# Kernel tuning notes

Hardware: AMD Instinct MI355X
Metric: run time of the kernel (lower is better)

The kernel has to match this reference:

```python
import jax, jax.numpy as jnp
import numpy as np

B, T, IN_DIM, EMB = 8, 2048, 1024, 1024
NEG_INF = -1e30  # stand-in for float('-inf'); exp() underflows to 0 identically


def setup_inputs() -> dict:
    key = jax.random.key(0)
    ks = jax.random.split(key, 7)
    s = 1.0 / np.sqrt(IN_DIM)
    return {
        "x": jax.random.normal(ks[0], (B, T, IN_DIM), dtype=jnp.float32),
        "Wq": jax.random.normal(ks[1], (IN_DIM, EMB), dtype=jnp.float32) * s,
        "bq": jax.random.normal(ks[2], (EMB,), dtype=jnp.float32) * 0.01,
        "Wk": jax.random.normal(ks[3], (IN_DIM, EMB), dtype=jnp.float32) * s,
        "bk": jax.random.normal(ks[4], (EMB,), dtype=jnp.float32) * 0.01,
        "Wv": jax.random.normal(ks[5], (IN_DIM, EMB), dtype=jnp.float32) * s,
        "bv": jax.random.normal(ks[6], (EMB,), dtype=jnp.float32) * 0.01,
    }


def reference(x, Wq, bq, Wk, bk, Wv, bv):
    # projections: [B, T, EMB]
    q = x @ Wq + bq
    k = x @ Wk + bk
    v = x @ Wv + bv
    scale = jnp.asarray(EMB, x.dtype) ** 0.5
    # scores: [B, T, T]
    scores = jnp.einsum("btd,bsd->bts", q, k) / scale
    Tq = scores.shape[-2]
    causal = jnp.tril(jnp.ones((Tq, Tq), dtype=bool))  # [T, T]
    scores = jnp.where(causal, scores, jnp.asarray(NEG_INF, scores.dtype))
    # Faithful to torch.vmap(softmax): per-batch GLOBAL-matrix softmax
    # (max and sum taken over the whole [T, T] matrix, not per row).
    m = jnp.max(scores, axis=(-2, -1), keepdims=True)
    e = jnp.exp(scores - m)
    w = e / jnp.sum(e, axis=(-2, -1), keepdims=True)
    # output: [B, T, EMB]
    return jnp.einsum("bts,bsd->btd", w, v)
```

## Files before the change

### kernel.cpp

```cpp
#include <hip/hip_runtime.h>
#include <stdint.h>


#define B_   8
#define T_   2048
#define DIM  1024

typedef _Float16 f16;
typedef f16   f16x8 __attribute__((ext_vector_type(8)));
typedef f16   f16x4 __attribute__((ext_vector_type(4)));
typedef float f32x4 __attribute__((ext_vector_type(4)));

typedef const __attribute__((address_space(1))) void gvoid_t;
typedef __attribute__((address_space(3))) void lvoid_t;


__device__ __forceinline__ void stage_half256(const uint16_t* __restrict__ g, int ld,
                                              uint16_t* s, int tid) {
#pragma unroll
  for (int j = 0; j < 2; ++j) {
    int r   = j * 64 + (tid >> 3);
    int seg = (tid & 7) ^ (r & 7);
    const uint16_t* gp = g + (size_t)r * ld + seg * 8;
    uint16_t* sp = s + j * 4096 + (tid >> 6) * 512;
    __builtin_amdgcn_global_load_lds((gvoid_t*)gp, (lvoid_t*)sp, 16, 0, 0);
  }
}

__device__ __forceinline__ f16x8 frag64(const uint16_t* s, int r, int gseg) {
  return *(const f16x8*)(s + r * 64 + ((gseg ^ (r & 7)) * 8));
}

__device__ __forceinline__ void lda4(const uint16_t* s, int rbase, int quad, int l15,
                                     f16x8 o[4][2]) {
#pragma unroll
  for (int mf = 0; mf < 4; ++mf) {
    int r = rbase + mf * 16 + l15;
#pragma unroll
    for (int kk = 0; kk < 2; ++kk) o[mf][kk] = frag64(s, r, kk * 4 + quad);
  }
}

__device__ __forceinline__ void ldb2(const uint16_t* s, int rbase, int quad, int l15,
                                     f16x8 o[2][2]) {
#pragma unroll
  for (int nf = 0; nf < 2; ++nf) {
    int r = rbase + nf * 16 + l15;
#pragma unroll
    for (int kk = 0; kk < 2; ++kk) o[nf][kk] = frag64(s, r, kk * 4 + quad);
  }
}

__device__ __forceinline__ void ldb1(const uint16_t* s, int rbase, int quad, int l15,
                                     f16x8 o[2]) {
  int r = rbase + l15;
#pragma unroll
  for (int kk = 0; kk < 2; ++kk) o[kk] = frag64(s, r, kk * 4 + quad);
}

template <int M0, int N0>
__device__ __forceinline__ void mm16(f16x8 a[4][2], f16x8 b[2][2], f32x4 (&acc)[8][4]) {
#pragma unroll
  for (int kk = 0; kk < 2; ++kk)
#pragma unroll
    for (int mf = 0; mf < 4; ++mf)
#pragma unroll
      for (int nf = 0; nf < 2; ++nf)
        acc[M0 + mf][N0 + nf] = __builtin_amdgcn_mfma_f32_16x16x32_f16(
            a[mf][kk], b[nf][kk], acc[M0 + mf][N0 + nf], 0, 0, 0);
}

template <int M0, int N0>
__device__ __forceinline__ void mm8(f16x8 a[4][2], f16x8 b[2], f32x4 (&acc)[8][2]) {
#pragma unroll
  for (int kk = 0; kk < 2; ++kk)
#pragma unroll
    for (int mf = 0; mf < 4; ++mf)
      acc[M0 + mf][N0] = __builtin_amdgcn_mfma_f32_16x16x32_f16(
          a[mf][kk], b[kk], acc[M0 + mf][N0], 0, 0, 0);
}

#define SYNC_MFMA(AA, BB, M0, N0)                      \
  __builtin_amdgcn_s_barrier();                        \
  asm volatile("s_waitcnt lgkmcnt(0)" ::: "memory");   \
  __builtin_amdgcn_s_setprio(1);                       \
  mm16<M0, N0>(AA, BB, acc);                           \
  __builtin_amdgcn_s_setprio(0);                       \
  __builtin_amdgcn_s_barrier();

#define SYNC_MFMA8(AA, BB, M0, N0)                     \
  __builtin_amdgcn_s_barrier();                        \
  asm volatile("s_waitcnt lgkmcnt(0)" ::: "memory");   \
  __builtin_amdgcn_s_setprio(1);                       \
  mm8<M0, N0>(AA, BB, acc);                            \
  __builtin_amdgcn_s_setprio(0);                       \
  __builtin_amdgcn_s_barrier();

__device__ __forceinline__ void gemm256_8ph(const uint16_t* __restrict__ gA,
                                            const uint16_t* __restrict__ gB,
                                            int lda, int ldb, int nIter,
                                            uint16_t* smem, f32x4 (&acc)[8][4]) {
  const int tid = threadIdx.x, lane = tid & 63;
  const int quad = lane >> 4, l15 = lane & 15;
  const int wv = tid >> 6, wr = wv >> 2, wc = wv & 3;

  uint16_t* sA0 = smem;
  uint16_t* sA1 = smem + 16384;
  uint16_t* sB0 = smem + 32768;
  uint16_t* sB1 = smem + 49152;

  stage_half256(gA,                          lda, sA0,        tid);
  stage_half256(gA + 128 * (size_t)lda,      lda, sA0 + 8192, tid);
  stage_half256(gB,                          ldb, sB0,        tid);
  stage_half256(gB + 128 * (size_t)ldb,      ldb, sB0 + 8192, tid);
  stage_half256(gB + 64,                     ldb, sB1,        tid);
  stage_half256(gB + 64 + 128 * (size_t)ldb, ldb, sB1 + 8192, tid);
  asm volatile("s_waitcnt vmcnt(4)" ::: "memory");
  __builtin_amdgcn_s_barrier();

  f16x8 alo[4][2], ahi[4][2], blo[2][2], bhi[2][2];
#pragma unroll 1
  for (int it = 0; it < nIter - 1; ++it) {
    const int t1 = 2 * it + 1, t2 = 2 * it + 2, t3 = 2 * it + 3;
    const uint16_t* gA1 = gA + t1 * 64;
    const uint16_t* gA2 = gA + t2 * 64;
    const uint16_t* gB2 = gB + t2 * 64;
    const uint16_t* gB3 = gB + t3 * 64;

    lda4(sA0, wr * 128,      quad, l15, alo);
    ldb2(sB0, wc * 64,       quad, l15, blo);
    stage_half256(gA1, lda, sA1, tid);
    SYNC_MFMA(alo, blo, 0, 0)
    ldb2(sB0, wc * 64 + 32,  quad, l15, bhi);
    stage_half256(gA1 + 128 * (size_t)lda, lda, sA1 + 8192, tid);
    SYNC_MFMA(alo, bhi, 0, 2)
    lda4(sA0, wr * 128 + 64, quad, l15, ahi);
    stage_half256(gB2, ldb, sB0, tid);
    SYNC_MFMA(ahi, bhi, 4, 2)
    stage_half256(gB2 + 128 * (size_t)ldb, ldb, sB0 + 8192, tid);
    asm volatile("s_waitcnt vmcnt(4)" ::: "memory");
    SYNC_MFMA(ahi, blo, 4, 0)
    lda4(sA1, wr * 128,      quad, l15, alo);
    ldb2(sB1, wc * 64,       quad, l15, blo);
    stage_half256(gA2, lda, sA0, tid);
    SYNC_MFMA(alo, blo, 0, 0)
    ldb2(sB1, wc * 64 + 32,  quad, l15, bhi);
    stage_half256(gA2 + 128 * (size_t)lda, lda, sA0 + 8192, tid);
    SYNC_MFMA(alo, bhi, 0, 2)
    lda4(sA1, wr * 128 + 64, quad, l15, ahi);
    stage_half256(gB3, ldb, sB1, tid);
    SYNC_MFMA(ahi, bhi, 4, 2)
    stage_half256(gB3 + 128 * (size_t)ldb, ldb, sB1 + 8192, tid);
    asm volatile("s_waitcnt vmcnt(4)" ::: "memory");
    SYNC_MFMA(ahi, blo, 4, 0)
  }

  {
    const uint16_t* gA1 = gA + (2 * nIter - 1) * 64;
    lda4(sA0, wr * 128,      quad, l15, alo);
    ldb2(sB0, wc * 64,       quad, l15, blo);
    stage_half256(gA1, lda, sA1, tid);
    SYNC_MFMA(alo, blo, 0, 0)
    ldb2(sB0, wc * 64 + 32,  quad, l15, bhi);
    stage_half256(gA1 + 128 * (size_t)lda, lda, sA1 + 8192, tid);
    SYNC_MFMA(alo, bhi, 0, 2)
    lda4(sA0, wr * 128 + 64, quad, l15, ahi);
    SYNC_MFMA(ahi, bhi, 4, 2)
    asm volatile("s_waitcnt vmcnt(0)" ::: "memory");
    SYNC_MFMA(ahi, blo, 4, 0)
    lda4(sA1, wr * 128,      quad, l15, alo);
    ldb2(sB1, wc * 64,       quad, l15, blo);
    SYNC_MFMA(alo, blo, 0, 0)
    ldb2(sB1, wc * 64 + 32,  quad, l15, bhi);
    SYNC_MFMA(alo, bhi, 0, 2)
    lda4(sA1, wr * 128 + 64, quad, l15, ahi);
    SYNC_MFMA(ahi, bhi, 4, 2)
    SYNC_MFMA(ahi, blo, 4, 0)
  }
}

__device__ __forceinline__ void gemm256n128_8ph(const uint16_t* __restrict__ gA,
                                                const uint16_t* __restrict__ gB,
                                                int lda, int ldb, int nIter,
                                                uint16_t* smem, f32x4 (&acc)[8][2]) {
  const int tid = threadIdx.x, lane = tid & 63;
  const int quad = lane >> 4, l15 = lane & 15;
  const int wv = tid >> 6, wr = wv >> 2, wc = wv & 3;

  uint16_t* sA0 = smem;
  uint16_t* sA1 = smem + 16384;
  uint16_t* sB0 = smem + 32768;
  uint16_t* sB1 = smem + 40960;

  stage_half256(gA,                     lda, sA0,        tid);
  stage_half256(gA + 128 * (size_t)lda, lda, sA0 + 8192, tid);
  stage_half256(gB,                     ldb, sB0,        tid);
  stage_half256(gB + 64,                ldb, sB1,        tid);
  asm volatile("s_waitcnt vmcnt(2)" ::: "memory");
  __builtin_amdgcn_s_barrier();

  f16x8 alo[4][2], ahi[4][2], b0[2], b1[2];
#pragma unroll 1
  for (int it = 0; it < nIter - 1; ++it) {
    const int t1 = 2 * it + 1, t2 = 2 * it + 2, t3 = 2 * it + 3;
    const uint16_t* gA1 = gA + t1 * 64;
    const uint16_t* gA2 = gA + t2 * 64;

    lda4(sA0, wr * 128,      quad, l15, alo);
    ldb1(sB0, wc * 32,       quad, l15, b0);
    stage_half256(gA1, lda, sA1, tid);
    SYNC_MFMA8(alo, b0, 0, 0)
    ldb1(sB0, wc * 32 + 16,  quad, l15, b1);
    stage_half256(gA1 + 128 * (size_t)lda, lda, sA1 + 8192, tid);
    SYNC_MFMA8(alo, b1, 0, 1)
    lda4(sA0, wr * 128 + 64, quad, l15, ahi);
    stage_half256(gB + t2 * 64, ldb, sB0, tid);
    SYNC_MFMA8(ahi, b1, 4, 1)
    asm volatile("s_waitcnt vmcnt(2)" ::: "memory");
    SYNC_MFMA8(ahi, b0, 4, 0)
    lda4(sA1, wr * 128,      quad, l15, alo);
    ldb1(sB1, wc * 32,       quad, l15, b0);
    stage_half256(gA2, lda, sA0, tid);
    SYNC_MFMA8(alo, b0, 0, 0)
    ldb1(sB1, wc * 32 + 16,  quad, l15, b1);
    stage_half256(gA2 + 128 * (size_t)lda, lda, sA0 + 8192, tid);
    SYNC_MFMA8(alo, b1, 0, 1)
    lda4(sA1, wr * 128 + 64, quad, l15, ahi);
    stage_half256(gB + t3 * 64, ldb, sB1, tid);
    SYNC_MFMA8(ahi, b1, 4, 1)
    asm volatile("s_waitcnt vmcnt(2)" ::: "memory");
    SYNC_MFMA8(ahi, b0, 4, 0)
  }

  {
    const uint16_t* gA1 = gA + (2 * nIter - 1) * 64;
    lda4(sA0, wr * 128,      quad, l15, alo);
    ldb1(sB0, wc * 32,       quad, l15, b0);
    stage_half256(gA1, lda, sA1, tid);
    SYNC_MFMA8(alo, b0, 0, 0)
    ldb1(sB0, wc * 32 + 16,  quad, l15, b1);
    stage_half256(gA1 + 128 * (size_t)lda, lda, sA1 + 8192, tid);
    SYNC_MFMA8(alo, b1, 0, 1)
    lda4(sA0, wr * 128 + 64, quad, l15, ahi);
    SYNC_MFMA8(ahi, b1, 4, 1)
    asm volatile("s_waitcnt vmcnt(0)" ::: "memory");
    SYNC_MFMA8(ahi, b0, 4, 0)
    lda4(sA1, wr * 128,      quad, l15, alo);
    ldb1(sB1, wc * 32,       quad, l15, b0);
    SYNC_MFMA8(alo, b0, 0, 0)
    ldb1(sB1, wc * 32 + 16,  quad, l15, b1);
    SYNC_MFMA8(alo, b1, 0, 1)
    lda4(sA1, wr * 128 + 64, quad, l15, ahi);
    SYNC_MFMA8(ahi, b1, 4, 1)
    SYNC_MFMA8(ahi, b0, 4, 0)
  }
}

__device__ __forceinline__ void zero_acc8(f32x4 (&acc)[8][4]) {
  f32x4 z = {0.f, 0.f, 0.f, 0.f};
#pragma unroll
  for (int i = 0; i < 8; ++i)
#pragma unroll
    for (int j = 0; j < 4; ++j) acc[i][j] = z;
}


__global__ void zero_lrow_kernel(float* __restrict__ lrow) {
  lrow[blockIdx.x * 256 + threadIdx.x] = 0.f;
}

__global__ void conv_x_kernel(const float* __restrict__ x, f16* __restrict__ xf) {
  size_t i = (size_t)blockIdx.x * 256 + threadIdx.x;
  float4 v = ((const float4*)x)[i];
  f16x4 o = {(f16)v.x, (f16)v.y, (f16)v.z, (f16)v.w};
  ((f16x4*)xf)[i] = o;
}

__global__ void convT_w_kernel(const float* __restrict__ Wq, const float* __restrict__ Wk,
                               const float* __restrict__ Wv, f16* __restrict__ WT) {
  __shared__ float tile[64][65];
  const int z = blockIdx.z;
  const float* W = (z == 0) ? Wq : (z == 1) ? Wk : Wv;
  const int r0 = blockIdx.x * 64, c0 = blockIdx.y * 64, tid = threadIdx.x;
#pragma unroll
  for (int i = 0; i < 16; ++i) {
    int rr = (tid >> 6) + 4 * i, cc = tid & 63;
    tile[rr][cc] = W[(size_t)(r0 + rr) * DIM + c0 + cc];
  }
  __syncthreads();
#pragma unroll
  for (int i = 0; i < 16; ++i) {
    int nn = (tid >> 6) + 4 * i, kk = tid & 63;
    WT[(size_t)z * DIM * DIM + (size_t)(c0 + nn) * DIM + r0 + kk] = (f16)tile[kk][nn];
  }
}

__global__ void reduce_z_kernel(const float* __restrict__ lrow, float* __restrict__ invZ) {
  const int b = blockIdx.x, tid = threadIdx.x;
  float s = 0.f;
  for (int i = tid; i < T_; i += 256) s += lrow[(size_t)b * T_ + i];
#pragma unroll
  for (int off = 1; off < 64; off <<= 1) s += __shfl_xor(s, off, 64);
  __shared__ float red[4];
  if ((tid & 63) == 0) red[tid >> 6] = s;
  __syncthreads();
  if (tid == 0) invZ[b] = 1.0f / (red[0] + red[1] + red[2] + red[3]);
}


__global__ __launch_bounds__(512, 2) void proj_kernel(
    const f16* __restrict__ xf, const f16* __restrict__ WT,
    const float* __restrict__ bq, const float* __restrict__ bk, const float* __restrict__ bv,
    f16* __restrict__ q, f16* __restrict__ k, f16* __restrict__ vT) {
  __shared__ uint16_t smem[65536];

  const int bid = blockIdx.x;
  const int xcd = bid & 7, local = bid >> 3;
  const int bx = xcd * 8 + (local & 7);
  const int zy = local >> 3;
  const int z = zy >> 2, by = zy & 3;
  const size_t arow = (size_t)bx * 256;
  const int    bcol = by * 256;

  f32x4 acc[8][4];
  zero_acc8(acc);
  gemm256_8ph((const uint16_t*)xf + arow * DIM,
              (const uint16_t*)WT + (size_t)z * DIM * DIM + (size_t)bcol * DIM,
              DIM, DIM, 8, smem, acc);

  const float* bias = (z == 0) ? bq : (z == 1) ? bk : bv;
  const int tid = threadIdx.x, lane = tid & 63, wv = tid >> 6;
  const int quad = lane >> 4, l15 = lane & 15;
  const int wr = wv >> 2, wc = wv & 3;
  if (z < 2) {
    f16* O = z ? k : q;
#pragma unroll
    for (int mf = 0; mf < 8; ++mf)
#pragma unroll
      for (int nf = 0; nf < 4; ++nf) {
        int n = bcol + wc * 64 + nf * 16 + l15;
        float bb = bias[n];
        size_t row0 = arow + wr * 128 + mf * 16 + quad * 4;
#pragma unroll
        for (int r = 0; r < 4; ++r)
          O[(row0 + r) * DIM + n] = (f16)(acc[mf][nf][r] + bb);
      }
  } else {
#pragma unroll
    for (int mf = 0; mf < 8; ++mf)
#pragma unroll
      for (int nf = 0; nf < 4; ++nf) {
        int n = bcol + wc * 64 + nf * 16 + l15;
        float bb = bias[n];
        int row0 = (int)arow + wr * 128 + mf * 16 + quad * 4;
        int bb_i = row0 >> 11, t0 = row0 & 2047;
        f16x4 pk;
#pragma unroll
        for (int r = 0; r < 4; ++r) pk[r] = (f16)(acc[mf][nf][r] + bb);
        *(f16x4*)(vT + ((size_t)bb_i * DIM + n) * T_ + t0) = pk;
      }
  }
}

__global__ __launch_bounds__(512, 2) void scores_kernel(
    const f16* __restrict__ q, const f16* __restrict__ k,
    f16* __restrict__ E, float* __restrict__ lrow) {
  __shared__ uint16_t smem[65536];
  const int bid = blockIdx.x;
  const int b = bid & 7, tri = bid >> 3;
  int qi = 0;
  while ((qi + 1) * (qi + 2) / 2 <= tri) ++qi;
  const int ki = tri - qi * (qi + 1) / 2;

  f32x4 acc[8][4];
  zero_acc8(acc);
  gemm256_8ph((const uint16_t*)(q + ((size_t)b * T_ + qi * 256) * DIM),
              (const uint16_t*)(k + ((size_t)b * T_ + ki * 256) * DIM),
              DIM, DIM, 8, smem, acc);

  const int tid = threadIdx.x, lane = tid & 63, wv = tid >> 6;
  const int quad = lane >> 4, l15 = lane & 15;
  const int wr = wv >> 2, wc = wv & 3;
  f16*   Eb = E + (size_t)b * T_ * T_;
  float* lb = lrow + (size_t)b * T_;
  const bool diag = (ki == qi);
#pragma unroll
  for (int mf = 0; mf < 8; ++mf) {
    float rs[4] = {0.f, 0.f, 0.f, 0.f};
#pragma unroll
    for (int nf = 0; nf < 4; ++nf)
#pragma unroll
      for (int r = 0; r < 4; ++r) {
        int t = qi * 256 + wr * 128 + mf * 16 + quad * 4 + r;
        int s = ki * 256 + wc * 64 + nf * 16 + l15;
        float e = 0.f;
        if (!diag || s <= t) e = __expf(fminf(acc[mf][nf][r] * 0.03125f, 11.f));
        Eb[(size_t)t * T_ + s] = (f16)e;
        rs[r] += e;
      }
#pragma unroll
    for (int off = 1; off < 16; off <<= 1)
#pragma unroll
      for (int r = 0; r < 4; ++r) rs[r] += __shfl_xor(rs[r], off, 64);
    if (l15 == 0)
#pragma unroll
      for (int r = 0; r < 4; ++r)
        atomicAdd(&lb[qi * 256 + wr * 128 + mf * 16 + quad * 4 + r], rs[r]);
  }
}

__global__ __launch_bounds__(512, 2) void pv_kernel(
    const f16* __restrict__ E, const f16* __restrict__ vT,
    const float* __restrict__ invZ, float* __restrict__ out) {
  __shared__ uint16_t smem[49152];
  const int bid = blockIdx.x;
  const int b = bid & 7, local = bid >> 3;
  const int nt = local & 7, pair = local >> 3;

  const float iz = invZ[b];
  const int tid = threadIdx.x, lane = tid & 63, wv = tid >> 6;
  const int quad = lane >> 4, l15 = lane & 15;
  const int wr = wv >> 2, wc = wv & 3;
  float* ob = out + (size_t)b * T_ * DIM;
  const uint16_t* Bv = (const uint16_t*)(vT + ((size_t)b * DIM + nt * 128) * (size_t)T_);

#pragma unroll 1
  for (int j = 0; j < 2; ++j) {
    const int qi = j ? (7 - pair) : pair;
    f32x4 acc[8][2];
    {
      f32x4 z = {0.f, 0.f, 0.f, 0.f};
#pragma unroll
      for (int i = 0; i < 8; ++i) { acc[i][0] = z; acc[i][1] = z; }
    }
    gemm256n128_8ph((const uint16_t*)(E + ((size_t)b * T_ + qi * 256) * (size_t)T_),
                    Bv, T_, T_, (qi + 1) * 2, smem, acc);
#pragma unroll
    for (int mf = 0; mf < 8; ++mf)
#pragma unroll
      for (int nf = 0; nf < 2; ++nf)
#pragma unroll
        for (int r = 0; r < 4; ++r) {
          int t = qi * 256 + wr * 128 + mf * 16 + quad * 4 + r;
          int n = nt * 128 + wc * 32 + nf * 16 + l15;
          ob[(size_t)t * DIM + n] = acc[mf][nf][r] * iz;
        }
  }
}


extern "C" void kernel_launch(void* const* d_in, const int* in_sizes, int n_in,
                              void* d_out, int out_size, void* d_ws, size_t ws_size,
                              hipStream_t stream) {
  const float* x  = (const float*)d_in[0];
  const float* Wq = (const float*)d_in[1];
  const float* bq = (const float*)d_in[2];
  const float* Wk = (const float*)d_in[3];
  const float* bk = (const float*)d_in[4];
  const float* Wv = (const float*)d_in[5];
  const float* bv = (const float*)d_in[6];
  float* out = (float*)d_out;

  char* ws = (char*)d_ws;
  f16*   E    = (f16*)ws;
  f16*   xf   = (f16*)ws;
  f16*   q    = (f16*)(ws + 67108864);
  f16*   k    = (f16*)(ws + 100663296);
  f16*   vT   = (f16*)(ws + 134217728);
  f16*   WT   = (f16*)(ws + 167772160);
  float* lrow = (float*)(ws + 174063616);
  float* invZ = (float*)(ws + 174129152);
  if (ws_size < (size_t)174129184) return;

  zero_lrow_kernel<<<64, 256, 0, stream>>>(lrow);
  conv_x_kernel<<<16384, 256, 0, stream>>>(x, xf);
  convT_w_kernel<<<dim3(16, 16, 3), 256, 0, stream>>>(Wq, Wk, Wv, WT);
  proj_kernel<<<dim3(768), 512, 0, stream>>>(xf, WT, bq, bk, bv, q, k, vT);
  scores_kernel<<<dim3(288), 512, 0, stream>>>(q, k, E, lrow);
  reduce_z_kernel<<<B_, 256, 0, stream>>>(lrow, invZ);
  pv_kernel<<<dim3(256), 512, 0, stream>>>(E, vT, invZ, out);
}
```

Baseline: 346.7 us.

## Retile projection GEMM to 128x256 BK32 tiles and split scores into half-width jobs

```diff
diff --git a/kernel.cpp b/kernel.cpp
--- a/kernel.cpp
+++ b/kernel.cpp
@@ -13,7 +13,6 @@
 
 typedef const __attribute__((address_space(1))) void gvoid_t;
 typedef __attribute__((address_space(3))) void lvoid_t;
-
 
 __device__ __forceinline__ void stage_half256(const uint16_t* __restrict__ g, int ld,
                                               uint16_t* s, int tid) {
@@ -31,6 +30,19 @@
   return *(const f16x8*)(s + r * 64 + ((gseg ^ (r & 7)) * 8));
 }
 
+__device__ __forceinline__ void stage_u8k(const uint16_t* __restrict__ g, int ld,
+                                          uint16_t* s, int tid) {
+  int r   = tid >> 2;
+  int seg = (tid & 3) ^ (r & 3);
+  const uint16_t* gp = g + (size_t)r * ld + seg * 8;
+  uint16_t* sp = s + (tid >> 6) * 512;
+  __builtin_amdgcn_global_load_lds((gvoid_t*)gp, (lvoid_t*)sp, 16, 0, 0);
+}
+
+__device__ __forceinline__ f16x8 frag32(const uint16_t* s, int r, int gseg) {
+  return *(const f16x8*)(s + r * 32 + ((gseg ^ (r & 3)) * 8));
+}
+
 __device__ __forceinline__ void lda4(const uint16_t* s, int rbase, int quad, int l15,
                                      f16x8 o[4][2]) {
 #pragma unroll
@@ -38,16 +50,6 @@
     int r = rbase + mf * 16 + l15;
 #pragma unroll
     for (int kk = 0; kk < 2; ++kk) o[mf][kk] = frag64(s, r, kk * 4 + quad);
-  }
-}
-
-__device__ __forceinline__ void ldb2(const uint16_t* s, int rbase, int quad, int l15,
-                                     f16x8 o[2][2]) {
-#pragma unroll
-  for (int nf = 0; nf < 2; ++nf) {
-    int r = rbase + nf * 16 + l15;
-#pragma unroll
-    for (int kk = 0; kk < 2; ++kk) o[nf][kk] = frag64(s, r, kk * 4 + quad);
   }
 }
 
@@ -58,16 +60,16 @@
   for (int kk = 0; kk < 2; ++kk) o[kk] = frag64(s, r, kk * 4 + quad);
 }
 
-template <int M0, int N0>
-__device__ __forceinline__ void mm16(f16x8 a[4][2], f16x8 b[2][2], f32x4 (&acc)[8][4]) {
-#pragma unroll
-  for (int kk = 0; kk < 2; ++kk)
-#pragma unroll
-    for (int mf = 0; mf < 4; ++mf)
-#pragma unroll
-      for (int nf = 0; nf < 2; ++nf)
-        acc[M0 + mf][N0 + nf] = __builtin_amdgcn_mfma_f32_16x16x32_f16(
-            a[mf][kk], b[nf][kk], acc[M0 + mf][N0 + nf], 0, 0, 0);
+__device__ __forceinline__ void lda4q(const uint16_t* s, int rbase, int quad, int l15,
+                                      f16x8 o[4]) {
+#pragma unroll
+  for (int mf = 0; mf < 4; ++mf) o[mf] = frag32(s, rbase + mf * 16 + l15, quad);
+}
+
+__device__ __forceinline__ void ldb2q(const uint16_t* s, int rbase, int quad, int l15,
+                                      f16x8 o[2]) {
+#pragma unroll
+  for (int nf = 0; nf < 2; ++nf) o[nf] = frag32(s, rbase + nf * 16 + l15, quad);
 }
 
 template <int M0, int N0>
@@ -80,13 +82,15 @@
           a[mf][kk], b[kk], acc[M0 + mf][N0], 0, 0, 0);
 }
 
-#define SYNC_MFMA(AA, BB, M0, N0)                      \
-  __builtin_amdgcn_s_barrier();                        \
-  asm volatile("s_waitcnt lgkmcnt(0)" ::: "memory");   \
-  __builtin_amdgcn_s_setprio(1);                       \
-  mm16<M0, N0>(AA, BB, acc);                           \
-  __builtin_amdgcn_s_setprio(0);                       \
-  __builtin_amdgcn_s_barrier();
+template <int N0>
+__device__ __forceinline__ void mm8q(f16x8 a[4], f16x8 b[2], f32x4 (&acc)[4][4]) {
+#pragma unroll
+  for (int mf = 0; mf < 4; ++mf)
+#pragma unroll
+    for (int nf = 0; nf < 2; ++nf)
+      acc[mf][N0 + nf] = __builtin_amdgcn_mfma_f32_16x16x32_f16(
+          a[mf], b[nf], acc[mf][N0 + nf], 0, 0, 0);
+}
 
 #define SYNC_MFMA8(AA, BB, M0, N0)                     \
   __builtin_amdgcn_s_barrier();                        \
@@ -96,86 +100,73 @@
   __builtin_amdgcn_s_setprio(0);                       \
   __builtin_amdgcn_s_barrier();
 
-__device__ __forceinline__ void gemm256_8ph(const uint16_t* __restrict__ gA,
-                                            const uint16_t* __restrict__ gB,
-                                            int lda, int ldb, int nIter,
-                                            uint16_t* smem, f32x4 (&acc)[8][4]) {
+#define SYNC_MFMA8Q(AA, BB, N0)                        \
+  __builtin_amdgcn_s_barrier();                        \
+  asm volatile("s_waitcnt lgkmcnt(0)" ::: "memory");   \
+  __builtin_amdgcn_s_setprio(1);                       \
+  mm8q<N0>(AA, BB, acc);                               \
+  __builtin_amdgcn_s_setprio(0);                       \
+  __builtin_amdgcn_s_barrier();
+
+__device__ __forceinline__ void gemm128x256_bk32(const uint16_t* __restrict__ gA,
+                                                 const uint16_t* __restrict__ gB,
+                                                 int lda, int ldb, int nTiles,
+                                                 uint16_t* smem, f32x4 (&acc)[4][4]) {
   const int tid = threadIdx.x, lane = tid & 63;
   const int quad = lane >> 4, l15 = lane & 15;
   const int wv = tid >> 6, wr = wv >> 2, wc = wv & 3;
 
   uint16_t* sA0 = smem;
-  uint16_t* sA1 = smem + 16384;
-  uint16_t* sB0 = smem + 32768;
-  uint16_t* sB1 = smem + 49152;
-
-  stage_half256(gA,                          lda, sA0,        tid);
-  stage_half256(gA + 128 * (size_t)lda,      lda, sA0 + 8192, tid);
-  stage_half256(gB,                          ldb, sB0,        tid);
-  stage_half256(gB + 128 * (size_t)ldb,      ldb, sB0 + 8192, tid);
-  stage_half256(gB + 64,                     ldb, sB1,        tid);
-  stage_half256(gB + 64 + 128 * (size_t)ldb, ldb, sB1 + 8192, tid);
-  asm volatile("s_waitcnt vmcnt(4)" ::: "memory");
+  uint16_t* sA1 = smem + 4096;
+  uint16_t* sB0 = smem + 8192;
+  uint16_t* sB1 = smem + 16384;
+
+  stage_u8k(gA,                          lda, sA0,        tid);
+  stage_u8k(gB,                          ldb, sB0,        tid);
+  stage_u8k(gB + 128 * (size_t)ldb,      ldb, sB0 + 4096, tid);
+  stage_u8k(gA + 32,                     lda, sA1,        tid);
+  asm volatile("s_waitcnt vmcnt(1)" ::: "memory");
   __builtin_amdgcn_s_barrier();
 
-  f16x8 alo[4][2], ahi[4][2], blo[2][2], bhi[2][2];
+  f16x8 a[4], b0[2], b1[2];
 #pragma unroll 1
-  for (int it = 0; it < nIter - 1; ++it) {
-    const int t1 = 2 * it + 1, t2 = 2 * it + 2, t3 = 2 * it + 3;
-    const uint16_t* gA1 = gA + t1 * 64;
-    const uint16_t* gA2 = gA + t2 * 64;
-    const uint16_t* gB2 = gB + t2 * 64;
-    const uint16_t* gB3 = gB + t3 * 64;
-
-    lda4(sA0, wr * 128,      quad, l15, alo);
-    ldb2(sB0, wc * 64,       quad, l15, blo);
-    stage_half256(gA1, lda, sA1, tid);
-    SYNC_MFMA(alo, blo, 0, 0)
-    ldb2(sB0, wc * 64 + 32,  quad, l15, bhi);
-    stage_half256(gA1 + 128 * (size_t)lda, lda, sA1 + 8192, tid);
-    SYNC_MFMA(alo, bhi, 0, 2)
-    lda4(sA0, wr * 128 + 64, quad, l15, ahi);
-    stage_half256(gB2, ldb, sB0, tid);
-    SYNC_MFMA(ahi, bhi, 4, 2)
-    stage_half256(gB2 + 128 * (size_t)ldb, ldb, sB0 + 8192, tid);
-    asm volatile("s_waitcnt vmcnt(4)" ::: "memory");
-    SYNC_MFMA(ahi, blo, 4, 0)
-    lda4(sA1, wr * 128,      quad, l15, alo);
-    ldb2(sB1, wc * 64,       quad, l15, blo);
-    stage_half256(gA2, lda, sA0, tid);
-    SYNC_MFMA(alo, blo, 0, 0)
-    ldb2(sB1, wc * 64 + 32,  quad, l15, bhi);
-    stage_half256(gA2 + 128 * (size_t)lda, lda, sA0 + 8192, tid);
-    SYNC_MFMA(alo, bhi, 0, 2)
-    lda4(sA1, wr * 128 + 64, quad, l15, ahi);
-    stage_half256(gB3, ldb, sB1, tid);
-    SYNC_MFMA(ahi, bhi, 4, 2)
-    stage_half256(gB3 + 128 * (size_t)ldb, ldb, sB1 + 8192, tid);
-    asm volatile("s_waitcnt vmcnt(4)" ::: "memory");
-    SYNC_MFMA(ahi, blo, 4, 0)
-  }
-
+  for (int it = 0; it < nTiles / 2 - 1; ++it) {
+    const uint16_t* gAn = gA + (2 * it + 2) * 32;
+    const uint16_t* gBn = gB + (2 * it + 1) * 32;
+    lda4q(sA0, wr * 64,      quad, l15, a);
+    ldb2q(sB0, wc * 64,      quad, l15, b0);
+    stage_u8k(gBn,                     ldb, sB1,        tid);
+    stage_u8k(gBn + 128 * (size_t)ldb, ldb, sB1 + 4096, tid);
+    SYNC_MFMA8Q(a, b0, 0)
+    ldb2q(sB0, wc * 64 + 32, quad, l15, b1);
+    stage_u8k(gAn, lda, sA0, tid);
+    asm volatile("s_waitcnt vmcnt(1)" ::: "memory");
+    SYNC_MFMA8Q(a, b1, 2)
+    lda4q(sA1, wr * 64,      quad, l15, a);
+    ldb2q(sB1, wc * 64,      quad, l15, b0);
+    stage_u8k(gBn + 32,                     ldb, sB0,        tid);
+    stage_u8k(gBn + 32 + 128 * (size_t)ldb, ldb, sB0 + 4096, tid);
+    SYNC_MFMA8Q(a, b0, 0)
+    ldb2q(sB1, wc * 64 + 32, quad, l15, b1);
+    stage_u8k(gAn + 32, lda, sA1, tid);
+    asm volatile("s_waitcnt vmcnt(1)" ::: "memory");
+    SYNC_MFMA8Q(a, b1, 2)
+  }
   {
-    const uint16_t* gA1 = gA + (2 * nIter - 1) * 64;
-    lda4(sA0, wr * 128,      quad, l15, alo);
-    ldb2(sB0, wc * 64,       quad, l15, blo);
-    stage_half256(gA1, lda, sA1, tid);
-    SYNC_MFMA(alo, blo, 0, 0)
-    ldb2(sB0, wc * 64 + 32,  quad, l15, bhi);
-    stage_half256(gA1 + 128 * (size_t)lda, lda, sA1 + 8192, tid);
-    SYNC_MFMA(alo, bhi, 0, 2)
-    lda4(sA0, wr * 128 + 64, quad, l15, ahi);
-    SYNC_MFMA(ahi, bhi, 4, 2)
+    const uint16_t* gBn = gB + (nTiles - 1) * 32;
+    lda4q(sA0, wr * 64,      quad, l15, a);
+    ldb2q(sB0, wc * 64,      quad, l15, b0);
+    stage_u8k(gBn,                     ldb, sB1,        tid);
+    stage_u8k(gBn + 128 * (size_t)ldb, ldb, sB1 + 4096, tid);
+    SYNC_MFMA8Q(a, b0, 0)
+    ldb2q(sB0, wc * 64 + 32, quad, l15, b1);
     asm volatile("s_waitcnt vmcnt(0)" ::: "memory");
-    SYNC_MFMA(ahi, blo, 4, 0)
-    lda4(sA1, wr * 128,      quad, l15, alo);
-    ldb2(sB1, wc * 64,       quad, l15, blo);
-    SYNC_MFMA(alo, blo, 0, 0)
-    ldb2(sB1, wc * 64 + 32,  quad, l15, bhi);
-    SYNC_MFMA(alo, bhi, 0, 2)
-    lda4(sA1, wr * 128 + 64, quad, l15, ahi);
-    SYNC_MFMA(ahi, bhi, 4, 2)
-    SYNC_MFMA(ahi, blo, 4, 0)
+    SYNC_MFMA8Q(a, b1, 2)
+    lda4q(sA1, wr * 64,      quad, l15, a);
+    ldb2q(sB1, wc * 64,      quad, l15, b0);
+    SYNC_MFMA8Q(a, b0, 0)
+    ldb2q(sB1, wc * 64 + 32, quad, l15, b1);
+    SYNC_MFMA8Q(a, b1, 2)
   }
 }
 
@@ -231,7 +222,6 @@
     asm volatile("s_waitcnt vmcnt(2)" ::: "memory");
     SYNC_MFMA8(ahi, b0, 4, 0)
   }
-
   {
     const uint16_t* gA1 = gA + (2 * nIter - 1) * 64;
     lda4(sA0, wr * 128,      quad, l15, alo);
@@ -256,14 +246,6 @@
   }
 }
 
-__device__ __forceinline__ void zero_acc8(f32x4 (&acc)[8][4]) {
-  f32x4 z = {0.f, 0.f, 0.f, 0.f};
-#pragma unroll
-  for (int i = 0; i < 8; ++i)
-#pragma unroll
-    for (int j = 0; j < 4; ++j) acc[i][j] = z;
-}
-
 
 __global__ void zero_lrow_kernel(float* __restrict__ lrow) {
   lrow[blockIdx.x * 256 + threadIdx.x] = 0.f;
@@ -308,25 +290,31 @@
 }
 
 
-__global__ __launch_bounds__(512, 2) void proj_kernel(
+__global__ __launch_bounds__(512, 4) void proj_kernel(
     const f16* __restrict__ xf, const f16* __restrict__ WT,
     const float* __restrict__ bq, const float* __restrict__ bk, const float* __restrict__ bv,
     f16* __restrict__ q, f16* __restrict__ k, f16* __restrict__ vT) {
-  __shared__ uint16_t smem[65536];
+  __shared__ uint16_t smem[24576];
 
   const int bid = blockIdx.x;
   const int xcd = bid & 7, local = bid >> 3;
-  const int bx = xcd * 8 + (local & 7);
-  const int zy = local >> 3;
+  const int bxl = local / 12, zy = local % 12;
+  const int bx = xcd * 16 + bxl;
   const int z = zy >> 2, by = zy & 3;
-  const size_t arow = (size_t)bx * 256;
+  const size_t arow = (size_t)bx * 128;
   const int    bcol = by * 256;
 
-  f32x4 acc[8][4];
-  zero_acc8(acc);
-  gemm256_8ph((const uint16_t*)xf + arow * DIM,
-              (const uint16_t*)WT + (size_t)z * DIM * DIM + (size_t)bcol * DIM,
-              DIM, DIM, 8, smem, acc);
+  f32x4 acc[4][4];
+  {
+    f32x4 zz = {0.f, 0.f, 0.f, 0.f};
+#pragma unroll
+    for (int i = 0; i < 4; ++i)
+#pragma unroll
+      for (int j = 0; j < 4; ++j) acc[i][j] = zz;
+  }
+  gemm128x256_bk32((const uint16_t*)xf + arow * DIM,
+                   (const uint16_t*)WT + (size_t)z * DIM * DIM + (size_t)bcol * DIM,
+                   DIM, DIM, 32, smem, acc);
 
   const float* bias = (z == 0) ? bq : (z == 1) ? bk : bv;
   const int tid = threadIdx.x, lane = tid & 63, wv = tid >> 6;
@@ -335,24 +323,24 @@
   if (z < 2) {
     f16* O = z ? k : q;
 #pragma unroll
-    for (int mf = 0; mf < 8; ++mf)
+    for (int mf = 0; mf < 4; ++mf)
 #pragma unroll
       for (int nf = 0; nf < 4; ++nf) {
         int n = bcol + wc * 64 + nf * 16 + l15;
         float bb = bias[n];
-        size_t row0 = arow + wr * 128 + mf * 16 + quad * 4;
+        size_t row0 = arow + wr * 64 + mf * 16 + quad * 4;
 #pragma unroll
         for (int r = 0; r < 4; ++r)
           O[(row0 + r) * DIM + n] = (f16)(acc[mf][nf][r] + bb);
       }
   } else {
 #pragma unroll
-    for (int mf = 0; mf < 8; ++mf)
+    for (int mf = 0; mf < 4; ++mf)
 #pragma unroll
       for (int nf = 0; nf < 4; ++nf) {
         int n = bcol + wc * 64 + nf * 16 + l15;
         float bb = bias[n];
-        int row0 = (int)arow + wr * 128 + mf * 16 + quad * 4;
+        int row0 = (int)arow + wr * 64 + mf * 16 + quad * 4;
         int bb_i = row0 >> 11, t0 = row0 & 2047;
         f16x4 pk;
 #pragma unroll
@@ -365,47 +353,56 @@
 __global__ __launch_bounds__(512, 2) void scores_kernel(
     const f16* __restrict__ q, const f16* __restrict__ k,
     f16* __restrict__ E, float* __restrict__ lrow) {
-  __shared__ uint16_t smem[65536];
+  __shared__ uint16_t smem[49152];
   const int bid = blockIdx.x;
-  const int b = bid & 7, tri = bid >> 3;
-  int qi = 0;
-  while ((qi + 1) * (qi + 2) / 2 <= tri) ++qi;
-  const int ki = tri - qi * (qi + 1) / 2;
-
-  f32x4 acc[8][4];
-  zero_acc8(acc);
-  gemm256_8ph((const uint16_t*)(q + ((size_t)b * T_ + qi * 256) * DIM),
-              (const uint16_t*)(k + ((size_t)b * T_ + ki * 256) * DIM),
-              DIM, DIM, 8, smem, acc);
+  const int b = bid & 7, blk = bid >> 3;
 
   const int tid = threadIdx.x, lane = tid & 63, wv = tid >> 6;
   const int quad = lane >> 4, l15 = lane & 15;
   const int wr = wv >> 2, wc = wv & 3;
   f16*   Eb = E + (size_t)b * T_ * T_;
   float* lb = lrow + (size_t)b * T_;
-  const bool diag = (ki == qi);
-#pragma unroll
-  for (int mf = 0; mf < 8; ++mf) {
-    float rs[4] = {0.f, 0.f, 0.f, 0.f};
-#pragma unroll
-    for (int nf = 0; nf < 4; ++nf)
-#pragma unroll
-      for (int r = 0; r < 4; ++r) {
-        int t = qi * 256 + wr * 128 + mf * 16 + quad * 4 + r;
-        int s = ki * 256 + wc * 64 + nf * 16 + l15;
-        float e = 0.f;
-        if (!diag || s <= t) e = __expf(fminf(acc[mf][nf][r] * 0.03125f, 11.f));
-        Eb[(size_t)t * T_ + s] = (f16)e;
-        rs[r] += e;
-      }
-#pragma unroll
-    for (int off = 1; off < 16; off <<= 1)
-#pragma unroll
-      for (int r = 0; r < 4; ++r) rs[r] += __shfl_xor(rs[r], off, 64);
-    if (l15 == 0)
-#pragma unroll
-      for (int r = 0; r < 4; ++r)
-        atomicAdd(&lb[qi * 256 + wr * 128 + mf * 16 + quad * 4 + r], rs[r]);
+
+#pragma unroll 1
+  for (int jid = blk; jid < 72; jid += 32) {
+    int qi = 0;
+    while ((qi + 1) * (qi + 2) <= jid) ++qi;
+    const int h = jid - qi * (qi + 1);
+
+    f32x4 acc[8][2];
+    {
+      f32x4 zz = {0.f, 0.f, 0.f, 0.f};
+#pragma unroll
+      for (int i = 0; i < 8; ++i) { acc[i][0] = zz; acc[i][1] = zz; }
+    }
+    gemm256n128_8ph((const uint16_t*)(q + ((size_t)b * T_ + qi * 256) * DIM),
+                    (const uint16_t*)(k + ((size_t)b * T_ + h * 128) * DIM),
+                    DIM, DIM, 8, smem, acc);
+
+    const bool diag = (h >= 2 * qi);
+#pragma unroll
+    for (int mf = 0; mf < 8; ++mf) {
+      float rs[4] = {0.f, 0.f, 0.f, 0.f};
+#pragma unroll
+      for (int nf = 0; nf < 2; ++nf)
+#pragma unroll
+        for (int r = 0; r < 4; ++r) {
+          int t = qi * 256 + wr * 128 + mf * 16 + quad * 4 + r;
+          int s = h * 128 + wc * 32 + nf * 16 + l15;
+          float e = 0.f;
+          if (!diag || s <= t) e = __expf(fminf(acc[mf][nf][r] * 0.03125f, 11.f));
+          Eb[(size_t)t * T_ + s] = (f16)e;
+          rs[r] += e;
+        }
+#pragma unroll
+      for (int off = 1; off < 16; off <<= 1)
+#pragma unroll
+        for (int r = 0; r < 4; ++r) rs[r] += __shfl_xor(rs[r], off, 64);
+      if (l15 == 0)
+#pragma unroll
+        for (int r = 0; r < 4; ++r)
+          atomicAdd(&lb[qi * 256 + wr * 128 + mf * 16 + quad * 4 + r], rs[r]);
+    }
   }
 }
 
@@ -475,8 +472,8 @@
   zero_lrow_kernel<<<64, 256, 0, stream>>>(lrow);
   conv_x_kernel<<<16384, 256, 0, stream>>>(x, xf);
   convT_w_kernel<<<dim3(16, 16, 3), 256, 0, stream>>>(Wq, Wk, Wv, WT);
-  proj_kernel<<<dim3(768), 512, 0, stream>>>(xf, WT, bq, bk, bv, q, k, vT);
-  scores_kernel<<<dim3(288), 512, 0, stream>>>(q, k, E, lrow);
+  proj_kernel<<<dim3(1536), 512, 0, stream>>>(xf, WT, bq, bk, bv, q, k, vT);
+  scores_kernel<<<dim3(256), 512, 0, stream>>>(q, k, E, lrow);
   reduce_z_kernel<<<B_, 256, 0, stream>>>(lrow, invZ);
   pv_kernel<<<dim3(256), 512, 0, stream>>>(E, vT, invZ, out);
 }
```

Result: slower. 366.3 us (+5.6%).

## Replace 8-phase GEMM mainloop with triple-buffered single-barrier K=32 pipeline

Applied to the files above, without the earlier changes.

```diff
diff --git a/kernel.cpp b/kernel.cpp
--- a/kernel.cpp
+++ b/kernel.cpp
@@ -13,7 +13,6 @@
 
 typedef const __attribute__((address_space(1))) void gvoid_t;
 typedef __attribute__((address_space(3))) void lvoid_t;
-
 
 __device__ __forceinline__ void stage_half256(const uint16_t* __restrict__ g, int ld,
                                               uint16_t* s, int tid) {
@@ -31,6 +30,19 @@
   return *(const f16x8*)(s + r * 64 + ((gseg ^ (r & 7)) * 8));
 }
 
+__device__ __forceinline__ void stage_u8k(const uint16_t* __restrict__ g, int ld,
+                                          uint16_t* s, int tid) {
+  int r   = tid >> 2;
+  int seg = (tid & 3) ^ ((r >> 1) & 3);
+  const uint16_t* gp = g + (size_t)r * ld + seg * 8;
+  uint16_t* sp = s + (tid >> 6) * 512;
+  __builtin_amdgcn_global_load_lds((gvoid_t*)gp, (lvoid_t*)sp, 16, 0, 0);
+}
+
+__device__ __forceinline__ f16x8 frag32(const uint16_t* s, int r, int gseg) {
+  return *(const f16x8*)(s + r * 32 + ((gseg ^ ((r >> 1) & 3)) * 8));
+}
+
 __device__ __forceinline__ void lda4(const uint16_t* s, int rbase, int quad, int l15,
                                      f16x8 o[4][2]) {
 #pragma unroll
@@ -38,16 +50,6 @@
     int r = rbase + mf * 16 + l15;
 #pragma unroll
     for (int kk = 0; kk < 2; ++kk) o[mf][kk] = frag64(s, r, kk * 4 + quad);
-  }
-}
-
-__device__ __forceinline__ void ldb2(const uint16_t* s, int rbase, int quad, int l15,
-                                     f16x8 o[2][2]) {
-#pragma unroll
-  for (int nf = 0; nf < 2; ++nf) {
-    int r = rbase + nf * 16 + l15;
-#pragma unroll
-    for (int kk = 0; kk < 2; ++kk) o[nf][kk] = frag64(s, r, kk * 4 + quad);
   }
 }
 
@@ -59,18 +61,6 @@
 }
 
 template <int M0, int N0>
-__device__ __forceinline__ void mm16(f16x8 a[4][2], f16x8 b[2][2], f32x4 (&acc)[8][4]) {
-#pragma unroll
-  for (int kk = 0; kk < 2; ++kk)
-#pragma unroll
-    for (int mf = 0; mf < 4; ++mf)
-#pragma unroll
-      for (int nf = 0; nf < 2; ++nf)
-        acc[M0 + mf][N0 + nf] = __builtin_amdgcn_mfma_f32_16x16x32_f16(
-            a[mf][kk], b[nf][kk], acc[M0 + mf][N0 + nf], 0, 0, 0);
-}
-
-template <int M0, int N0>
 __device__ __forceinline__ void mm8(f16x8 a[4][2], f16x8 b[2], f32x4 (&acc)[8][2]) {
 #pragma unroll
   for (int kk = 0; kk < 2; ++kk)
@@ -79,14 +69,6 @@
       acc[M0 + mf][N0] = __builtin_amdgcn_mfma_f32_16x16x32_f16(
           a[mf][kk], b[kk], acc[M0 + mf][N0], 0, 0, 0);
 }
-
-#define SYNC_MFMA(AA, BB, M0, N0)                      \
-  __builtin_amdgcn_s_barrier();                        \
-  asm volatile("s_waitcnt lgkmcnt(0)" ::: "memory");   \
-  __builtin_amdgcn_s_setprio(1);                       \
-  mm16<M0, N0>(AA, BB, acc);                           \
-  __builtin_amdgcn_s_setprio(0);                       \
-  __builtin_amdgcn_s_barrier();
 
 #define SYNC_MFMA8(AA, BB, M0, N0)                     \
   __builtin_amdgcn_s_barrier();                        \
@@ -96,87 +78,67 @@
   __builtin_amdgcn_s_setprio(0);                       \
   __builtin_amdgcn_s_barrier();
 
-__device__ __forceinline__ void gemm256_8ph(const uint16_t* __restrict__ gA,
-                                            const uint16_t* __restrict__ gB,
-                                            int lda, int ldb, int nIter,
-                                            uint16_t* smem, f32x4 (&acc)[8][4]) {
+__device__ __forceinline__ void gemm256_1bar(const uint16_t* __restrict__ gA,
+                                             const uint16_t* __restrict__ gB,
+                                             int lda, int ldb, int nTiles,
+                                             uint16_t* smem, f32x4 (&acc)[8][4]) {
   const int tid = threadIdx.x, lane = tid & 63;
   const int quad = lane >> 4, l15 = lane & 15;
   const int wv = tid >> 6, wr = wv >> 2, wc = wv & 3;
 
-  uint16_t* sA0 = smem;
-  uint16_t* sA1 = smem + 16384;
-  uint16_t* sB0 = smem + 32768;
-  uint16_t* sB1 = smem + 49152;
-
-  stage_half256(gA,                          lda, sA0,        tid);
-  stage_half256(gA + 128 * (size_t)lda,      lda, sA0 + 8192, tid);
-  stage_half256(gB,                          ldb, sB0,        tid);
-  stage_half256(gB + 128 * (size_t)ldb,      ldb, sB0 + 8192, tid);
-  stage_half256(gB + 64,                     ldb, sB1,        tid);
-  stage_half256(gB + 64 + 128 * (size_t)ldb, ldb, sB1 + 8192, tid);
+#define STAGE_T(tt)                                                      \
+  { uint16_t* sa = smem + ((tt) % 3) * 8192;                             \
+    uint16_t* sb = smem + 24576 + ((tt) % 3) * 8192;                     \
+    const uint16_t* ga = gA + (tt) * 32;                                 \
+    const uint16_t* gb = gB + (tt) * 32;                                 \
+    stage_u8k(ga,                     lda, sa,        tid);              \
+    stage_u8k(ga + 128 * (size_t)lda, lda, sa + 4096, tid);              \
+    stage_u8k(gb,                     ldb, sb,        tid);              \
+    stage_u8k(gb + 128 * (size_t)ldb, ldb, sb + 4096, tid); }
+
+#define READS_T(tt)                                                      \
+  { const uint16_t* sa = smem + ((tt) % 3) * 8192;                       \
+    const uint16_t* sb = smem + 24576 + ((tt) % 3) * 8192;               \
+    _Pragma("unroll")                                                    \
+    for (int mf = 0; mf < 8; ++mf)                                       \
+      a[mf] = frag32(sa, wr * 128 + mf * 16 + l15, quad);                \
+    _Pragma("unroll")                                                    \
+    for (int nf = 0; nf < 4; ++nf)                                       \
+      b[nf] = frag32(sb, wc * 64 + nf * 16 + l15, quad); }
+
+#define MFMA_T                                                           \
+  __builtin_amdgcn_s_setprio(1);                                         \
+  _Pragma("unroll")                                                      \
+  for (int mf = 0; mf < 8; ++mf)                                         \
+    _Pragma("unroll")                                                    \
+    for (int nf = 0; nf < 4; ++nf)                                       \
+      acc[mf][nf] = __builtin_amdgcn_mfma_f32_16x16x32_f16(              \
+          a[mf], b[nf], acc[mf][nf], 0, 0, 0);                           \
+  __builtin_amdgcn_s_setprio(0);
+
+  STAGE_T(0)
+  STAGE_T(1)
   asm volatile("s_waitcnt vmcnt(4)" ::: "memory");
   __builtin_amdgcn_s_barrier();
 
-  f16x8 alo[4][2], ahi[4][2], blo[2][2], bhi[2][2];
+  f16x8 a[8], b[4];
 #pragma unroll 1
-  for (int it = 0; it < nIter - 1; ++it) {
-    const int t1 = 2 * it + 1, t2 = 2 * it + 2, t3 = 2 * it + 3;
-    const uint16_t* gA1 = gA + t1 * 64;
-    const uint16_t* gA2 = gA + t2 * 64;
-    const uint16_t* gB2 = gB + t2 * 64;
-    const uint16_t* gB3 = gB + t3 * 64;
-
-    lda4(sA0, wr * 128,      quad, l15, alo);
-    ldb2(sB0, wc * 64,       quad, l15, blo);
-    stage_half256(gA1, lda, sA1, tid);
-    SYNC_MFMA(alo, blo, 0, 0)
-    ldb2(sB0, wc * 64 + 32,  quad, l15, bhi);
-    stage_half256(gA1 + 128 * (size_t)lda, lda, sA1 + 8192, tid);
-    SYNC_MFMA(alo, bhi, 0, 2)
-    lda4(sA0, wr * 128 + 64, quad, l15, ahi);
-    stage_half256(gB2, ldb, sB0, tid);
-    SYNC_MFMA(ahi, bhi, 4, 2)
-    stage_half256(gB2 + 128 * (size_t)ldb, ldb, sB0 + 8192, tid);
+  for (int t = 0; t < nTiles - 2; ++t) {
+    STAGE_T(t + 2)
+    READS_T(t)
+    MFMA_T
+    __builtin_amdgcn_s_barrier();
     asm volatile("s_waitcnt vmcnt(4)" ::: "memory");
-    SYNC_MFMA(ahi, blo, 4, 0)
-    lda4(sA1, wr * 128,      quad, l15, alo);
-    ldb2(sB1, wc * 64,       quad, l15, blo);
-    stage_half256(gA2, lda, sA0, tid);
-    SYNC_MFMA(alo, blo, 0, 0)
-    ldb2(sB1, wc * 64 + 32,  quad, l15, bhi);
-    stage_half256(gA2 + 128 * (size_t)lda, lda, sA0 + 8192, tid);
-    SYNC_MFMA(alo, bhi, 0, 2)
-    lda4(sA1, wr * 128 + 64, quad, l15, ahi);
-    stage_half256(gB3, ldb, sB1, tid);
-    SYNC_MFMA(ahi, bhi, 4, 2)
-    stage_half256(gB3 + 128 * (size_t)ldb, ldb, sB1 + 8192, tid);
-    asm volatile("s_waitcnt vmcnt(4)" ::: "memory");
-    SYNC_MFMA(ahi, blo, 4, 0)
-  }
-
-  {
-    const uint16_t* gA1 = gA + (2 * nIter - 1) * 64;
-    lda4(sA0, wr * 128,      quad, l15, alo);
-    ldb2(sB0, wc * 64,       quad, l15, blo);
-    stage_half256(gA1, lda, sA1, tid);
-    SYNC_MFMA(alo, blo, 0, 0)
-    ldb2(sB0, wc * 64 + 32,  quad, l15, bhi);
-    stage_half256(gA1 + 128 * (size_t)lda, lda, sA1 + 8192, tid);
-    SYNC_MFMA(alo, bhi, 0, 2)
-    lda4(sA0, wr * 128 + 64, quad, l15, ahi);
-    SYNC_MFMA(ahi, bhi, 4, 2)
-    asm volatile("s_waitcnt vmcnt(0)" ::: "memory");
-    SYNC_MFMA(ahi, blo, 4, 0)
-    lda4(sA1, wr * 128,      quad, l15, alo);
-    ldb2(sB1, wc * 64,       quad, l15, blo);
-    SYNC_MFMA(alo, blo, 0, 0)
-    ldb2(sB1, wc * 64 + 32,  quad, l15, bhi);
-    SYNC_MFMA(alo, bhi, 0, 2)
-    lda4(sA1, wr * 128 + 64, quad, l15, ahi);
-    SYNC_MFMA(ahi, bhi, 4, 2)
-    SYNC_MFMA(ahi, blo, 4, 0)
-  }
+  }
+  READS_T(nTiles - 2)
+  MFMA_T
+  __builtin_amdgcn_s_barrier();
+  asm volatile("s_waitcnt vmcnt(0)" ::: "memory");
+  READS_T(nTiles - 1)
+  MFMA_T
+#undef STAGE_T
+#undef READS_T
+#undef MFMA_T
 }
 
 __device__ __forceinline__ void gemm256n128_8ph(const uint16_t* __restrict__ gA,
@@ -231,7 +193,6 @@
     asm volatile("s_waitcnt vmcnt(2)" ::: "memory");
     SYNC_MFMA8(ahi, b0, 4, 0)
   }
-
   {
     const uint16_t* gA1 = gA + (2 * nIter - 1) * 64;
     lda4(sA0, wr * 128,      quad, l15, alo);
@@ -312,7 +273,7 @@
     const f16* __restrict__ xf, const f16* __restrict__ WT,
     const float* __restrict__ bq, const float* __restrict__ bk, const float* __restrict__ bv,
     f16* __restrict__ q, f16* __restrict__ k, f16* __restrict__ vT) {
-  __shared__ uint16_t smem[65536];
+  __shared__ uint16_t smem[49152];
 
   const int bid = blockIdx.x;
   const int xcd = bid & 7, local = bid >> 3;
@@ -324,9 +285,9 @@
 
   f32x4 acc[8][4];
   zero_acc8(acc);
-  gemm256_8ph((const uint16_t*)xf + arow * DIM,
-              (const uint16_t*)WT + (size_t)z * DIM * DIM + (size_t)bcol * DIM,
-              DIM, DIM, 8, smem, acc);
+  gemm256_1bar((const uint16_t*)xf + arow * DIM,
+               (const uint16_t*)WT + (size_t)z * DIM * DIM + (size_t)bcol * DIM,
+               DIM, DIM, 32, smem, acc);
 
   const float* bias = (z == 0) ? bq : (z == 1) ? bk : bv;
   const int tid = threadIdx.x, lane = tid & 63, wv = tid >> 6;
@@ -365,7 +326,7 @@
 __global__ __launch_bounds__(512, 2) void scores_kernel(
     const f16* __restrict__ q, const f16* __restrict__ k,
     f16* __restrict__ E, float* __restrict__ lrow) {
-  __shared__ uint16_t smem[65536];
+  __shared__ uint16_t smem[49152];
   const int bid = blockIdx.x;
   const int b = bid & 7, tri = bid >> 3;
   int qi = 0;
@@ -374,9 +335,9 @@
 
   f32x4 acc[8][4];
   zero_acc8(acc);
-  gemm256_8ph((const uint16_t*)(q + ((size_t)b * T_ + qi * 256) * DIM),
-              (const uint16_t*)(k + ((size_t)b * T_ + ki * 256) * DIM),
-              DIM, DIM, 8, smem, acc);
+  gemm256_1bar((const uint16_t*)(q + ((size_t)b * T_ + qi * 256) * DIM),
+               (const uint16_t*)(k + ((size_t)b * T_ + ki * 256) * DIM),
+               DIM, DIM, 32, smem, acc);
 
   const int tid = threadIdx.x, lane = tid & 63, wv = tid >> 6;
   const int quad = lane >> 4, l15 = lane & 15;
```

After: 354.1 us. 1.02x slower.
